# Performance work log

Measured on AMD Instinct MI355X. Metric: run time of the kernel, lower is better.

## Reference

```python
import jax, jax.numpy as jnp
import numpy as np

B, S, U, H = 4, 2048, 1024, 8
HD = U // H
EPS = 1e-8


def setup_inputs() -> dict:
    key = jax.random.key(0)
    ks = jax.random.split(key, 10)
    sc = 1.0 / np.sqrt(U)
    x = jax.random.normal(ks[0], (B, S, U), dtype=jnp.float32)
    Wq = jax.random.normal(ks[1], (U, U), dtype=jnp.float32) * sc
    bq = jnp.zeros((U,), dtype=jnp.float32)
    Wk = jax.random.normal(ks[2], (U, U), dtype=jnp.float32) * sc
    bk = jnp.zeros((U,), dtype=jnp.float32)
    Wv = jax.random.normal(ks[3], (U, U), dtype=jnp.float32) * sc
    bv = jnp.zeros((U,), dtype=jnp.float32)
    Wr = jax.random.normal(ks[4], (U, U), dtype=jnp.float32) * sc
    br = jnp.zeros((U,), dtype=jnp.float32)
    gamma = jnp.ones((U,), dtype=jnp.float32)
    beta = jnp.zeros((U,), dtype=jnp.float32)
    return {"x": x, "Wq": Wq, "bq": bq, "Wk": Wk, "bk": bk, "Wv": Wv,
            "bv": bv, "Wr": Wr, "br": br, "gamma": gamma, "beta": beta}


def reference(x, Wq, bq, Wk, bk, Wv, bv, Wr, br, gamma, beta):
    relu = jax.nn.relu
    q = relu(jnp.einsum('bsu,uv->bsv', x, Wq) + bq)
    k = relu(jnp.einsum('bsu,uv->bsv', x, Wk) + bk)
    v = relu(jnp.einsum('bsu,uv->bsv', x, Wv) + bv)
    res = relu(jnp.einsum('bsu,uv->bsv', x, Wr) + br)
    # Faithful to the original: a raw reshape (NOT split+transpose head split).
    q = q.reshape(B * H, S, HD)
    k = k.reshape(B * H, S, HD)
    v = v.reshape(B * H, S, HD)
    scores = jnp.einsum('nqd,nkd->nqk', q, k) / jnp.sqrt(jnp.float32(HD))
    weights = jax.nn.softmax(scores, axis=-1)
    # dropout_rate = 0.0 -> identity
    attn = jnp.einsum('nqk,nkd->nqd', weights, v)
    attn = attn.reshape(B, S, U)
    out = relu(attn + res)
    # custom LayerNorm (biased variance, eps inside sqrt)
    mean = jnp.mean(out, axis=-1, keepdims=True)
    var = jnp.mean(jnp.square(out - mean), axis=-1, keepdims=True)
    normed = (out - mean) / jnp.sqrt(var + EPS)
    return gamma * normed + beta
```

## Files before the change

### kernel.cpp

```cpp
#include <hip/hip_runtime.h>

typedef _Float16 half8_t __attribute__((ext_vector_type(8)));
typedef _Float16 half4_t __attribute__((ext_vector_type(4)));
typedef float floatx4 __attribute__((ext_vector_type(4)));

#define S_LEN 2048
#define U_DIM 1024
#define HD 128
#define M_TOT 8192
#define NHEADS 32

__device__ __forceinline__ void stage16(void* lds_base, const void* g_lane, int lane) {
#if defined(__has_builtin) && __has_builtin(__builtin_amdgcn_global_load_lds)
    __builtin_amdgcn_global_load_lds(
        (const __attribute__((address_space(1))) unsigned int*)g_lane,
        (__attribute__((address_space(3))) unsigned int*)lds_base, 16, 0, 0);
#else
    *(float4*)((char*)lds_base + lane * 16) = *(const float4*)g_lane;
#endif
}

__global__ __launch_bounds__(256) void k_convert_x(const float* __restrict__ x,
                                                   _Float16* __restrict__ xh) {
    size_t i = (size_t)blockIdx.x * 256 + threadIdx.x;
    float4 v = ((const float4*)x)[i];
    half4_t h;
    h[0] = (_Float16)v.x; h[1] = (_Float16)v.y;
    h[2] = (_Float16)v.z; h[3] = (_Float16)v.w;
    ((half4_t*)xh)[i] = h;
}

__global__ __launch_bounds__(256) void k_transpose_w(const float* __restrict__ Wq,
                                                     const float* __restrict__ Wk,
                                                     const float* __restrict__ Wv,
                                                     const float* __restrict__ Wr,
                                                     _Float16* __restrict__ wt) {
    const int z = blockIdx.z;
    const float* W = (z == 0) ? Wq : (z == 1) ? Wk : (z == 2) ? Wv : Wr;
    _Float16* o = wt + (size_t)z * U_DIM * U_DIM;
    __shared__ float t[64][65];
    const int n0 = blockIdx.x * 64, k0 = blockIdx.y * 64;
    const int tid = threadIdx.x;
    for (int c = tid; c < 1024; c += 256) {
        int kk = c >> 4, nn = (c & 15) * 4;
        float4 v = *(const float4*)&W[(size_t)(k0 + kk) * U_DIM + n0 + nn];
        t[kk][nn] = v.x; t[kk][nn + 1] = v.y; t[kk][nn + 2] = v.z; t[kk][nn + 3] = v.w;
    }
    __syncthreads();
    for (int c = tid; c < 512; c += 256) {
        int nn = c >> 3, ks = (c & 7) * 8;
        half8_t h;
        for (int i = 0; i < 8; i++) h[i] = (_Float16)t[ks + i][nn];
        *(half8_t*)&o[(size_t)(n0 + nn) * U_DIM + k0 + ks] = h;
    }
}

__global__ __launch_bounds__(256) void k_qkvr_gemm(const _Float16* __restrict__ xh,
                                                   const _Float16* __restrict__ wt,
                                                   const float* __restrict__ bq,
                                                   const float* __restrict__ bk,
                                                   const float* __restrict__ bv,
                                                   const float* __restrict__ br,
                                                   _Float16* __restrict__ qh,
                                                   _Float16* __restrict__ kh,
                                                   _Float16* __restrict__ vh,
                                                   _Float16* __restrict__ resh) {
    const int z = blockIdx.z;
    const int m0 = blockIdx.x * 128;
    const int n0 = blockIdx.y * 128;
    const _Float16* wz = wt + (size_t)z * U_DIM * U_DIM;

    __shared__ __align__(16) char AsB[8192];
    __shared__ __align__(16) char BsB[8192];
    __shared__ __align__(16) _Float16 Cs[128][136];

    const int tid = threadIdx.x;
    const int wave = tid >> 6, lane = tid & 63;
    const int lrow = lane & 15, quad = lane >> 4;
    const int wm = (wave >> 1) * 64, wn = (wave & 1) * 64;

    floatx4 acc[4][4];
    for (int i = 0; i < 4; i++)
        for (int j = 0; j < 4; j++) acc[i][j] = (floatx4)0.0f;

    const char* xb = (const char*)xh;
    const char* wb = (const char*)wz;

    for (int k0 = 0; k0 < U_DIM; k0 += 32) {
        for (int t = 0; t < 2; t++) {
            int c = wave * 2 + t;
            stage16(AsB + c * 1024,
                    xb + (size_t)(m0 + c * 16 + lrow) * 2048 + k0 * 2 + quad * 16, lane);
            stage16(BsB + c * 1024,
                    wb + (size_t)(n0 + c * 16 + lrow) * 2048 + k0 * 2 + quad * 16, lane);
        }
        __syncthreads();
        half8_t af[4], bf[4];
        for (int i = 0; i < 4; i++)
            af[i] = *(const half8_t*)(AsB + ((wave >> 1) * 4 + i) * 1024 + lane * 16);
        for (int j = 0; j < 4; j++)
            bf[j] = *(const half8_t*)(BsB + ((wave & 1) * 4 + j) * 1024 + lane * 16);
        for (int i = 0; i < 4; i++)
            for (int j = 0; j < 4; j++)
                acc[i][j] = __builtin_amdgcn_mfma_f32_16x16x32_f16(af[i], bf[j], acc[i][j], 0, 0, 0);
        __syncthreads();
    }

    const float* bias = (z == 0) ? bq : (z == 1) ? bk : (z == 2) ? bv : br;
    _Float16* dst = (z == 0) ? qh : (z == 1) ? kh : (z == 2) ? vh : resh;

    for (int i = 0; i < 4; i++) {
        for (int j = 0; j < 4; j++) {
            int col = wn + j * 16 + lrow;
            float bcol = bias[n0 + col];
            for (int r = 0; r < 4; r++) {
                float v = acc[i][j][r] + bcol;
                Cs[wm + i * 16 + quad * 4 + r][col] = (_Float16)(v > 0.f ? v : 0.f);
            }
        }
    }
    __syncthreads();
    for (int c = tid; c < 2048; c += 256) {
        int row = c >> 4, seg = (c & 15) * 8;
        *(half8_t*)&dst[(size_t)(m0 + row) * U_DIM + n0 + seg] = *(half8_t*)&Cs[row][seg];
    }
}

__global__ __launch_bounds__(256) void k_transpose_v(const _Float16* __restrict__ vh,
                                                     _Float16* __restrict__ vt) {
    const int n = blockIdx.z;
    const int s0 = blockIdx.x * 64, d0 = blockIdx.y * 64;
    const _Float16* V = vh + (size_t)n * S_LEN * HD;
    _Float16* O = vt + (size_t)n * HD * S_LEN;
    __shared__ _Float16 t[64][72];
    const int tid = threadIdx.x;
    for (int c = tid; c < 512; c += 256) {
        int srow = c >> 3, off = (c & 7) * 8;
        *(half8_t*)&t[srow][off] = *(const half8_t*)&V[(size_t)(s0 + srow) * HD + d0 + off];
    }
    __syncthreads();
    for (int c = tid; c < 512; c += 256) {
        int drow = c >> 3, soff = (c & 7) * 8;
        half8_t h;
        for (int i = 0; i < 8; i++) h[i] = t[soff + i][drow];
        *(half8_t*)&O[(size_t)(d0 + drow) * S_LEN + s0 + soff] = h;
    }
}

__global__ __launch_bounds__(256, 2) void k_flash(const _Float16* __restrict__ qh,
                                                  const _Float16* __restrict__ kh,
                                                  const _Float16* __restrict__ vt,
                                                  _Float16* __restrict__ attnh) {
    const int head = blockIdx.x + 8 * (blockIdx.y & 3);
    const int m0 = (int)(blockIdx.y >> 2) * 128;
    const _Float16* Q = qh + (size_t)head * S_LEN * HD;
    const char* Kb = (const char*)(kh + (size_t)head * S_LEN * HD);
    const char* Vb = (const char*)(vt + (size_t)head * HD * S_LEN);

    __shared__ __align__(16) char smem[51200];
    _Float16* Ps = (_Float16*)(smem + 32768);

    const int tid = threadIdx.x;
    const int w = tid >> 6, lane = tid & 63;
    const int lrow = lane & 15, quad = lane >> 4;

    half8_t qf[2][4];
    for (int i = 0; i < 2; i++)
        for (int k0 = 0; k0 < 4; k0++)
            qf[i][k0] = *(const half8_t*)&Q[(size_t)(m0 + w * 32 + i * 16 + lrow) * HD + k0 * 32 + quad * 8];

    floatx4 acc_o[2][8];
    for (int i = 0; i < 2; i++)
        for (int j = 0; j < 8; j++) acc_o[i][j] = (floatx4)0.0f;
    float lp[2] = {0.0f, 0.0f};

    const float C1 = 0.12751742f;

    for (int kt = 0; kt < 32; ++kt) {
        if (kt) __syncthreads();
        for (int t = 0; t < 4; t++) {
            int c = w * 4 + t;
            int k0 = c >> 2, j = c & 3;
            stage16(smem + c * 1024,
                    Kb + (size_t)(kt * 64 + j * 16 + lrow) * 256 + k0 * 64 + quad * 16, lane);
        }
        for (int t = 0; t < 4; t++) {
            int c = w * 4 + t;
            int k0s = c >> 3, dg = c & 7;
            stage16(smem + 16384 + c * 1024,
                    Vb + (size_t)(dg * 16 + lrow) * 4096 + kt * 128 + k0s * 64 + quad * 16, lane);
        }
        __syncthreads();

        floatx4 acc_t[2][4];
        for (int i = 0; i < 2; i++)
            for (int j = 0; j < 4; j++) acc_t[i][j] = (floatx4)0.0f;
        for (int k0 = 0; k0 < 4; k0++)
            for (int j = 0; j < 4; j++) {
                half8_t kf = *(const half8_t*)(smem + (k0 * 4 + j) * 1024 + lane * 16);
                for (int i = 0; i < 2; i++)
                    acc_t[i][j] = __builtin_amdgcn_mfma_f32_16x16x32_f16(kf, qf[i][k0], acc_t[i][j], 0, 0, 0);
            }

        for (int i = 0; i < 2; i++)
            for (int j = 0; j < 4; j++) {
                half4_t ph;
                for (int r = 0; r < 4; r++) {
                    float p = exp2f(fmaf(acc_t[i][j][r], C1, -6.0f));
                    lp[i] += p;
                    ph[r] = (_Float16)p;
                }
                *(half4_t*)&Ps[(w * 32 + i * 16 + lrow) * 72 + j * 16 + quad * 4] = ph;
            }

        for (int k0s = 0; k0s < 2; k0s++) {
            half8_t af[2];
            for (int i = 0; i < 2; i++)
                af[i] = *(const half8_t*)&Ps[(w * 32 + i * 16 + lrow) * 72 + k0s * 32 + quad * 8];
            for (int j = 0; j < 8; j++) {
                half8_t bv = *(const half8_t*)(smem + 16384 + (k0s * 8 + j) * 1024 + lane * 16);
                for (int i = 0; i < 2; i++)
                    acc_o[i][j] = __builtin_amdgcn_mfma_f32_16x16x32_f16(af[i], bv, acc_o[i][j], 0, 0, 0);
            }
        }
    }

    float inv[2][4];
    for (int i = 0; i < 2; i++) {
        lp[i] += __shfl_xor(lp[i], 16, 64);
        lp[i] += __shfl_xor(lp[i], 32, 64);
        for (int r = 0; r < 4; r++)
            inv[i][r] = 1.0f / __shfl(lp[i], quad * 4 + r, 64);
    }

    __syncthreads();
    _Float16* Os = (_Float16*)smem;
    for (int i = 0; i < 2; i++)
        for (int j = 0; j < 8; j++)
            for (int r = 0; r < 4; r++)
                Os[(w * 32 + i * 16 + quad * 4 + r) * 136 + j * 16 + lrow] =
                    (_Float16)(acc_o[i][j][r] * inv[i][r]);
    __syncthreads();
    const size_t base = (size_t)head * S_LEN * HD;
    for (int c = tid; c < 2048; c += 256) {
        int row = c >> 4, seg = (c & 15) * 8;
        *(half8_t*)&attnh[base + (size_t)(m0 + row) * HD + seg] = *(half8_t*)&Os[row * 136 + seg];
    }
}

__global__ __launch_bounds__(256) void k_ln(const _Float16* __restrict__ attnh,
                                            const _Float16* __restrict__ resh,
                                            const float* __restrict__ gamma,
                                            const float* __restrict__ beta,
                                            float* __restrict__ out) {
    const size_t row = blockIdx.x;
    const int tid = threadIdx.x;
    half4_t av = ((const half4_t*)(attnh + row * U_DIM))[tid];
    half4_t rv = ((const half4_t*)(resh + row * U_DIM))[tid];
    float o[4];
    float s1 = 0.f, s2 = 0.f;
    for (int i = 0; i < 4; i++) {
        o[i] = fmaxf((float)av[i] + (float)rv[i], 0.f);
        s1 += o[i];
        s2 += o[i] * o[i];
    }
    for (int off = 32; off; off >>= 1) {
        s1 += __shfl_xor(s1, off, 64);
        s2 += __shfl_xor(s2, off, 64);
    }
    __shared__ float red[8];
    const int wv = tid >> 6;
    if ((tid & 63) == 0) { red[wv] = s1; red[4 + wv] = s2; }
    __syncthreads();
    float ts1 = red[0] + red[1] + red[2] + red[3];
    float ts2 = red[4] + red[5] + red[6] + red[7];
    float mean = ts1 * (1.0f / 1024.0f);
    float var = ts2 * (1.0f / 1024.0f) - mean * mean;
    float rstd = rsqrtf(var + 1e-8f);
    float4 gv = ((const float4*)gamma)[tid];
    float4 bv = ((const float4*)beta)[tid];
    float4 ov;
    ov.x = gv.x * (o[0] - mean) * rstd + bv.x;
    ov.y = gv.y * (o[1] - mean) * rstd + bv.y;
    ov.z = gv.z * (o[2] - mean) * rstd + bv.z;
    ov.w = gv.w * (o[3] - mean) * rstd + bv.w;
    ((float4*)(out + row * U_DIM))[tid] = ov;
}

extern "C" void kernel_launch(void* const* d_in, const int* in_sizes, int n_in,
                              void* d_out, int out_size, void* d_ws, size_t ws_size,
                              hipStream_t stream) {
    const float* x     = (const float*)d_in[0];
    const float* Wq    = (const float*)d_in[1];
    const float* bq    = (const float*)d_in[2];
    const float* Wk    = (const float*)d_in[3];
    const float* bk    = (const float*)d_in[4];
    const float* Wv    = (const float*)d_in[5];
    const float* bv    = (const float*)d_in[6];
    const float* Wr    = (const float*)d_in[7];
    const float* br    = (const float*)d_in[8];
    const float* gamma = (const float*)d_in[9];
    const float* beta  = (const float*)d_in[10];
    float* out = (float*)d_out;

    char* p = (char*)d_ws;
    _Float16* xh = (_Float16*)p;    p += (size_t)M_TOT * U_DIM * 2;
    _Float16* wt = (_Float16*)p;    p += (size_t)4 * U_DIM * U_DIM * 2;
    _Float16* qh = (_Float16*)p;    p += (size_t)M_TOT * U_DIM * 2;
    _Float16* kh = (_Float16*)p;    p += (size_t)M_TOT * U_DIM * 2;
    _Float16* vh = (_Float16*)p;    p += (size_t)M_TOT * U_DIM * 2;
    _Float16* vt = (_Float16*)p;    p += (size_t)M_TOT * U_DIM * 2;
    _Float16* resh  = (_Float16*)p; p += (size_t)M_TOT * U_DIM * 2;
    _Float16* attnh = (_Float16*)p;

    k_convert_x<<<8192, 256, 0, stream>>>(x, xh);
    k_transpose_w<<<dim3(16, 16, 4), 256, 0, stream>>>(Wq, Wk, Wv, Wr, wt);
    k_qkvr_gemm<<<dim3(64, 8, 4), 256, 0, stream>>>(xh, wt, bq, bk, bv, br, qh, kh, vh, resh);
    k_transpose_v<<<dim3(32, 2, 32), 256, 0, stream>>>(vh, vt);
    k_flash<<<dim3(8, 64), 256, 0, stream>>>(qh, kh, vt, attnh);
    k_ln<<<8192, 256, 0, stream>>>(attnh, resh, gamma, beta, out);
}
```

Measured before the change: 355.2 us.

## Change LDS staging layout for coalesced rows and remap GEMM blocks per XCD

The LDS staging for the projection GEMM and the flash-attention K/V tiles now reads four lanes per row, giving 64 contiguous bytes per row from global memory instead of 16-byte pieces spread across 16 rows. An XOR swizzle on the 16-byte segment index keeps the MFMA fragment reads from LDS free of bank conflicts. The GEMM grid also moves to a 1D launch whose index mapping places blocks that share the same weight N-tile on the same XCD, aiming for better L2 reuse of weights. The risk is extra index arithmetic and a wrong swizzle mapping, which would corrupt the fragments.

After: 305.9 us. 1.16x faster.

```diff
diff --git a/kernel.cpp b/kernel.cpp
--- a/kernel.cpp
+++ b/kernel.cpp
@@ -19,6 +19,8 @@
     *(float4*)((char*)lds_base + lane * 16) = *(const float4*)g_lane;
 #endif
 }
+
+__device__ __forceinline__ int swz(int row) { return (row >> 1) & 3; }
 
 __global__ __launch_bounds__(256) void k_convert_x(const float* __restrict__ x,
                                                    _Float16* __restrict__ xh) {
@@ -65,9 +67,12 @@
                                                    _Float16* __restrict__ kh,
                                                    _Float16* __restrict__ vh,
                                                    _Float16* __restrict__ resh) {
-    const int z = blockIdx.z;
-    const int m0 = blockIdx.x * 128;
-    const int n0 = blockIdx.y * 128;
+    const int b = blockIdx.x;
+    const int xcd = b & 7, s = b >> 3;
+    const int pair = xcd + 8 * (s & 3);
+    const int m0 = (s >> 2) * 128;
+    const int n0 = (pair & 7) * 128;
+    const int z = pair >> 3;
     const _Float16* wz = wt + (size_t)z * U_DIM * U_DIM;
 
     __shared__ __align__(16) char AsB[8192];
@@ -78,6 +83,8 @@
     const int wave = tid >> 6, lane = tid & 63;
     const int lrow = lane & 15, quad = lane >> 4;
     const int wm = (wave >> 1) * 64, wn = (wave & 1) * 64;
+    const int lr4 = lane >> 2;
+    const int sseg = ((lane & 3) ^ swz(lr4)) * 16;
 
     floatx4 acc[4][4];
     for (int i = 0; i < 4; i++)
@@ -85,21 +92,22 @@
 
     const char* xb = (const char*)xh;
     const char* wb = (const char*)wz;
+    const int rsw = (quad ^ swz(lrow)) * 16;
 
     for (int k0 = 0; k0 < U_DIM; k0 += 32) {
         for (int t = 0; t < 2; t++) {
             int c = wave * 2 + t;
             stage16(AsB + c * 1024,
-                    xb + (size_t)(m0 + c * 16 + lrow) * 2048 + k0 * 2 + quad * 16, lane);
+                    xb + (size_t)(m0 + c * 16 + lr4) * 2048 + k0 * 2 + sseg, lane);
             stage16(BsB + c * 1024,
-                    wb + (size_t)(n0 + c * 16 + lrow) * 2048 + k0 * 2 + quad * 16, lane);
+                    wb + (size_t)(n0 + c * 16 + lr4) * 2048 + k0 * 2 + sseg, lane);
         }
         __syncthreads();
         half8_t af[4], bf[4];
         for (int i = 0; i < 4; i++)
-            af[i] = *(const half8_t*)(AsB + ((wave >> 1) * 4 + i) * 1024 + lane * 16);
+            af[i] = *(const half8_t*)(AsB + ((wave >> 1) * 4 + i) * 1024 + lrow * 64 + rsw);
         for (int j = 0; j < 4; j++)
-            bf[j] = *(const half8_t*)(BsB + ((wave & 1) * 4 + j) * 1024 + lane * 16);
+            bf[j] = *(const half8_t*)(BsB + ((wave & 1) * 4 + j) * 1024 + lrow * 64 + rsw);
         for (int i = 0; i < 4; i++)
             for (int j = 0; j < 4; j++)
                 acc[i][j] = __builtin_amdgcn_mfma_f32_16x16x32_f16(af[i], bf[j], acc[i][j], 0, 0, 0);
@@ -163,6 +171,9 @@
     const int tid = threadIdx.x;
     const int w = tid >> 6, lane = tid & 63;
     const int lrow = lane & 15, quad = lane >> 4;
+    const int lr4 = lane >> 2;
+    const int sseg = ((lane & 3) ^ swz(lr4)) * 16;
+    const int rsw = (quad ^ swz(lrow)) * 16;
 
     half8_t qf[2][4];
     for (int i = 0; i < 2; i++)
@@ -182,13 +193,13 @@
             int c = w * 4 + t;
             int k0 = c >> 2, j = c & 3;
             stage16(smem + c * 1024,
-                    Kb + (size_t)(kt * 64 + j * 16 + lrow) * 256 + k0 * 64 + quad * 16, lane);
+                    Kb + (size_t)(kt * 64 + j * 16 + lr4) * 256 + k0 * 64 + sseg, lane);
         }
         for (int t = 0; t < 4; t++) {
             int c = w * 4 + t;
             int k0s = c >> 3, dg = c & 7;
             stage16(smem + 16384 + c * 1024,
-                    Vb + (size_t)(dg * 16 + lrow) * 4096 + kt * 128 + k0s * 64 + quad * 16, lane);
+                    Vb + (size_t)(dg * 16 + lr4) * 4096 + kt * 128 + k0s * 64 + sseg, lane);
         }
         __syncthreads();
 
@@ -197,7 +208,7 @@
             for (int j = 0; j < 4; j++) acc_t[i][j] = (floatx4)0.0f;
         for (int k0 = 0; k0 < 4; k0++)
             for (int j = 0; j < 4; j++) {
-                half8_t kf = *(const half8_t*)(smem + (k0 * 4 + j) * 1024 + lane * 16);
+                half8_t kf = *(const half8_t*)(smem + (k0 * 4 + j) * 1024 + lrow * 64 + rsw);
                 for (int i = 0; i < 2; i++)
                     acc_t[i][j] = __builtin_amdgcn_mfma_f32_16x16x32_f16(kf, qf[i][k0], acc_t[i][j], 0, 0, 0);
             }
@@ -218,7 +229,7 @@
             for (int i = 0; i < 2; i++)
                 af[i] = *(const half8_t*)&Ps[(w * 32 + i * 16 + lrow) * 72 + k0s * 32 + quad * 8];
             for (int j = 0; j < 8; j++) {
-                half8_t bv = *(const half8_t*)(smem + 16384 + (k0s * 8 + j) * 1024 + lane * 16);
+                half8_t bv = *(const half8_t*)(smem + 16384 + (k0s * 8 + j) * 1024 + lrow * 64 + rsw);
                 for (int i = 0; i < 2; i++)
                     acc_o[i][j] = __builtin_amdgcn_mfma_f32_16x16x32_f16(af[i], bv, acc_o[i][j], 0, 0, 0);
             }
@@ -315,7 +326,7 @@
 
     k_convert_x<<<8192, 256, 0, stream>>>(x, xh);
     k_transpose_w<<<dim3(16, 16, 4), 256, 0, stream>>>(Wq, Wk, Wv, Wr, wt);
-    k_qkvr_gemm<<<dim3(64, 8, 4), 256, 0, stream>>>(xh, wt, bq, bk, bv, br, qh, kh, vh, resh);
+    k_qkvr_gemm<<<2048, 256, 0, stream>>>(xh, wt, bq, bk, bv, br, qh, kh, vh, resh);
     k_transpose_v<<<dim3(32, 2, 32), 256, 0, stream>>>(vh, vt);
     k_flash<<<dim3(8, 64), 256, 0, stream>>>(qh, kh, vt, attnh);
     k_ln<<<8192, 256, 0, stream>>>(attnh, resh, gamma, beta, out);
```
